# Kernel tuning notes

Hardware: AMD Instinct MI355X
Metric: run time of the kernel (lower is better)

Reference implementation:

```python
import jax, jax.numpy as jnp
import numpy as np

NEG_INF = -1e9  # mask fill value used by the original layer
LEAKY_SLOPE = 0.2


def setup_inputs() -> dict:
    key = jax.random.key(0)
    k1, k2, k3, k4 = jax.random.split(key, 4)
    B, N, D_in = 8, 1024, 256
    H, head_dim = 8, 32  # output_dim=256, concat_heads=True
    node_features = jax.random.normal(k1, (B, N, D_in), dtype=jnp.float32)
    adjacency = jax.random.randint(k2, (B, N, N), 0, 2, dtype=jnp.int32)
    W = jax.random.normal(k3, (H, D_in, head_dim), dtype=jnp.float32) * (1.0 / np.sqrt(D_in))
    a = jax.random.normal(k4, (H, 2 * head_dim), dtype=jnp.float32) * (1.0 / np.sqrt(2 * head_dim))
    bias = jnp.zeros((H * head_dim,), dtype=jnp.float32)
    return {"node_features": node_features, "adjacency": adjacency, "W": W, "a": a, "bias": bias}


def reference(node_features, adjacency, W, a, bias):
    # node_features: (B,N,D_in); adjacency: (B,N,N) in {0,1}
    H, _, hd = W.shape
    # Per-head linear transform: (B,H,N,head_dim)
    Wh = jnp.einsum('bni,hij->bhnj', node_features, W)
    # a @ concat(h_i, h_j) == a1 @ h_i + a2 @ h_j  (avoids O(N^2*2hd) concat)
    a1, a2 = a[:, :hd], a[:, hd:]
    e_i = jnp.einsum('bhnj,hj->bhn', Wh, a1)  # (B,H,N) source term
    e_j = jnp.einsum('bhnj,hj->bhn', Wh, a2)  # (B,H,N) target term
    scores = e_i[:, :, :, None] + e_j[:, :, None, :]  # (B,H,N,N)
    # LeakyReLU(0.2) exactly as ops.maximum(x, 0.2*x)
    scores = jnp.maximum(scores, LEAKY_SLOPE * scores)
    mask = adjacency.astype(scores.dtype)[:, None, :, :]  # (B,1,N,N)
    masked = scores * mask + (1.0 - mask) * NEG_INF
    attn = jax.nn.softmax(masked, axis=-1)  # (B,H,N,N)
    attended = jnp.einsum('bhij,bhjk->bhik', attn, Wh)  # (B,H,N,hd)
    B, _, N, _ = attended.shape
    # concat heads -> (B,N,H*hd); head order matches the python loop concat
    out = attended.transpose(0, 2, 1, 3).reshape(B, N, H * hd)
    out = out + bias
    return jax.nn.relu(out)
```

## Files before the change

### kernel.cpp

```cpp
#include <hip/hip_runtime.h>

#define GAT_B   8
#define GAT_N   1024
#define GAT_DIN 256
#define GAT_H   8
#define GAT_HD  32
#define GAT_LOG2E 1.4426950408889634f

typedef unsigned short gu16;
typedef unsigned int   gu32;
typedef __bf16 bf16x8 __attribute__((ext_vector_type(8)));
typedef __bf16 bf16x4 __attribute__((ext_vector_type(4)));
typedef float  f32x4v __attribute__((ext_vector_type(4)));

#if __has_builtin(__builtin_amdgcn_exp2f)
#define GAT_EXP2(x) __builtin_amdgcn_exp2f(x)
#else
#define GAT_EXP2(x) exp2f(x)
#endif

__device__ __forceinline__ float gb2f(gu16 u) { return __uint_as_float(((gu32)u) << 16); }

__device__ __forceinline__ void gat_detect(const gu16* p, int t, int* sflag) {
    if (t < 64) {
        int e0 = (p[2 * t]     >> 7) & 0xFF;
        int e1 = (p[2 * t + 1] >> 7) & 0xFF;
        unsigned long long m = __ballot((e0 >= 140) || (e1 >= 140));
        if (t == 0) *sflag = (m != 0ULL);
    }
}

__global__ __launch_bounds__(512) void CustomGATLayer_90348932038855_kernel(
    const void* __restrict__ Xv, const void* __restrict__ Wv, const void* __restrict__ Av,
    __bf16* __restrict__ whb, float* __restrict__ e1, float* __restrict__ e2)
{
    __shared__ __align__(16) __bf16 WlF[GAT_DIN * GAT_HD];
    __shared__ int sflag;

    const int t  = threadIdx.x;
    const int id = blockIdx.x;
    const int h  = id >> 5;
    const int mg = id & 31;

    gat_detect((const gu16*)Xv, t, &sflag);
    __syncthreads();
    const int fp32 = sflag;

    if (fp32) {
        const float* ws = (const float*)Wv + (size_t)h * GAT_DIN * GAT_HD;
        #pragma unroll
        for (int q = 0; q < 4; ++q) {
            int idx = q * 2048 + t * 4;
            int i = idx >> 5, k = idx & 31;
            float4 v = *(const float4*)(ws + idx);
            int d = (((i >> 5) * 32 + k) * 4 + ((i >> 3) & 3)) * 8 + (i & 7);
            WlF[d] = (__bf16)v.x; WlF[d + 32] = (__bf16)v.y;
            WlF[d + 64] = (__bf16)v.z; WlF[d + 96] = (__bf16)v.w;
        }
    } else {
        const gu16* ws = (const gu16*)Wv + (size_t)h * GAT_DIN * GAT_HD;
        gu16* wl = (gu16*)WlF;
        #pragma unroll
        for (int q = 0; q < 4; ++q) {
            int idx = q * 2048 + t * 4;
            int i = idx >> 5, k = idx & 31;
            ushort4 v = *(const ushort4*)(ws + idx);
            int d = (((i >> 5) * 32 + k) * 4 + ((i >> 3) & 3)) * 8 + (i & 7);
            wl[d] = v.x; wl[d + 32] = v.y; wl[d + 64] = v.z; wl[d + 96] = v.w;
        }
    }
    __syncthreads();

    const int wid = t >> 6, l = t & 63, g = l >> 4, c = l & 15;

    bf16x8 bf0[8], bf1[8];
    #pragma unroll
    for (int kc = 0; kc < 8; ++kc) {
        bf0[kc] = *(const bf16x8*)&WlF[((kc * 32 + c) * 4 + g) * 8];
        bf1[kc] = *(const bf16x8*)&WlF[((kc * 32 + c + 16) * 4 + g) * 8];
    }

    float a1c, a1c16, a2c, a2c16;
    if (fp32) {
        const float* ap = (const float*)Av + h * 2 * GAT_HD;
        a1c = ap[c] * GAT_LOG2E;      a1c16 = ap[c + 16] * GAT_LOG2E;
        a2c = ap[32 + c] * GAT_LOG2E; a2c16 = ap[48 + c] * GAT_LOG2E;
    } else {
        const gu16* ap = (const gu16*)Av + h * 2 * GAT_HD;
        a1c = gb2f(ap[c]) * GAT_LOG2E;      a1c16 = gb2f(ap[c + 16]) * GAT_LOG2E;
        a2c = gb2f(ap[32 + c]) * GAT_LOG2E; a2c16 = gb2f(ap[48 + c]) * GAT_LOG2E;
    }

    #pragma unroll
    for (int tt = 0; tt < 2; ++tt) {
        const int mt   = mg * 16 + wid * 2 + tt;
        const int M0   = mt * 16;
        const int b    = M0 >> 10;
        const int nloc = M0 & 1023;
        const int row  = nloc + c;

        f32x4v acc0 = {0.f, 0.f, 0.f, 0.f};
        f32x4v acc1 = {0.f, 0.f, 0.f, 0.f};

        if (fp32) {
            const float* xb = (const float*)Xv + ((size_t)b * GAT_N + row) * GAT_DIN;
            #pragma unroll
            for (int kc = 0; kc < 8; ++kc) {
                float4 x0 = *(const float4*)(xb + kc * 32 + 8 * g);
                float4 x1 = *(const float4*)(xb + kc * 32 + 8 * g + 4);
                bf16x8 af;
                af[0] = (__bf16)x0.x; af[1] = (__bf16)x0.y; af[2] = (__bf16)x0.z; af[3] = (__bf16)x0.w;
                af[4] = (__bf16)x1.x; af[5] = (__bf16)x1.y; af[6] = (__bf16)x1.z; af[7] = (__bf16)x1.w;
                acc0 = __builtin_amdgcn_mfma_f32_16x16x32_bf16(af, bf0[kc], acc0, 0, 0, 0);
                acc1 = __builtin_amdgcn_mfma_f32_16x16x32_bf16(af, bf1[kc], acc1, 0, 0, 0);
            }
        } else {
            const gu16* xb = (const gu16*)Xv + ((size_t)b * GAT_N + row) * GAT_DIN;
            #pragma unroll
            for (int kc = 0; kc < 8; ++kc) {
                bf16x8 af = *(const bf16x8*)(xb + kc * 32 + 8 * g);
                acc0 = __builtin_amdgcn_mfma_f32_16x16x32_bf16(af, bf0[kc], acc0, 0, 0, 0);
                acc1 = __builtin_amdgcn_mfma_f32_16x16x32_bf16(af, bf1[kc], acc1, 0, 0, 0);
            }
        }

        const int nb = nloc + 4 * g;
        const int jcc = nb >> 5, kg = (nb >> 3) & 3, e0 = nb & 7;
        const size_t fb = (((size_t)(b * GAT_H + h) * 32 + jcc) * 4 + kg) * 32;
        bf16x4 v0, v1;
        v0[0] = (__bf16)acc0[0]; v0[1] = (__bf16)acc0[1];
        v0[2] = (__bf16)acc0[2]; v0[3] = (__bf16)acc0[3];
        v1[0] = (__bf16)acc1[0]; v1[1] = (__bf16)acc1[1];
        v1[2] = (__bf16)acc1[2]; v1[3] = (__bf16)acc1[3];
        *(bf16x4*)(whb + (fb + c) * 8 + e0)      = v0;
        *(bf16x4*)(whb + (fb + c + 16) * 8 + e0) = v1;

        float p1[4], p2[4];
        #pragma unroll
        for (int q = 0; q < 4; ++q) {
            p1[q] = acc0[q] * a1c + acc1[q] * a1c16;
            p2[q] = acc0[q] * a2c + acc1[q] * a2c16;
            #pragma unroll
            for (int mm = 1; mm <= 8; mm <<= 1) {
                p1[q] += __shfl_xor(p1[q], mm);
                p2[q] += __shfl_xor(p2[q], mm);
            }
        }
        if (c == 0) {
            const size_t eb = (size_t)(b * GAT_H + h) * GAT_N + nb;
            #pragma unroll
            for (int q = 0; q < 4; ++q) { e1[eb + q] = p1[q]; e2[eb + q] = p2[q]; }
        }
    }
}

__global__ __launch_bounds__(512) void CustomGATLayer_90348932038855_attn(
    const void* __restrict__ Xv, const int* __restrict__ adj, const void* __restrict__ biasv,
    const __bf16* __restrict__ whb, const float* __restrict__ e1f, const float* __restrict__ e2f,
    float* __restrict__ out)
{
    __shared__ __align__(16) float e2l[GAT_H * GAT_N];
    __shared__ int sflag;

    const int t = threadIdx.x;
    const int h = t >> 6, l = t & 63, g = l >> 4, c = l & 15;
    const int id = blockIdx.x;
    const int b = id & 7, tile = id >> 3;
    const int i0 = tile * 16;

    gat_detect((const gu16*)Xv, t, &sflag);

    {
        const float* s = e2f + (size_t)(b * GAT_H + h) * GAT_N;
        float* d = e2l + h * GAT_N;
        #pragma unroll
        for (int q = 0; q < 4; ++q) {
            int off = (q * 64 + l) * 4;
            *(float4*)(d + off) = *(const float4*)(s + off);
        }
    }
    __syncthreads();
    const int fp32 = sflag;

    const float e1r = e1f[(size_t)(b * GAT_H + h) * GAT_N + i0 + c];
    const int* adjr = adj + ((size_t)(b * GAT_N + i0 + c)) * GAT_N + 8 * g;
    const __bf16* whr = whb + (size_t)(b * GAT_H + h) * (GAT_N * GAT_HD) + g * 256 + c * 8;
    const float* e2h = e2l + h * GAT_N + 8 * g;

    int4 aA0 = *(const int4*)(adjr),      aA1 = *(const int4*)(adjr + 4);
    int4 aB0 = *(const int4*)(adjr + 32), aB1 = *(const int4*)(adjr + 36);
    int4 aC0 = *(const int4*)(adjr + 64), aC1 = *(const int4*)(adjr + 68);
    bf16x8 wA0 = *(const bf16x8*)(whr),        wA1 = *(const bf16x8*)(whr + 128);
    bf16x8 wB0 = *(const bf16x8*)(whr + 1024), wB1 = *(const bf16x8*)(whr + 1152);

    f32x4v acc0 = {0.f, 0.f, 0.f, 0.f};
    f32x4v acc1 = {0.f, 0.f, 0.f, 0.f};
    f32x4v accS = {0.f, 0.f, 0.f, 0.f};
    bf16x8 onesf;
    #pragma unroll
    for (int e = 0; e < 8; ++e) onesf[e] = (__bf16)1.0f;

#define GAT_WCOMP(EV, AV, IDX) {                    \
        float s_ = e1r + (EV);                      \
        s_ = fmaxf(s_, 0.2f * s_);                  \
        s_ = fminf(s_, 86.0f);                      \
        float w_ = GAT_EXP2(s_);                    \
        w_ = (AV) ? w_ : 0.0f;                      \
        pf[IDX] = (__bf16)w_; }

    #pragma unroll 2
    for (int jc = 0; jc < 32; ++jc) {
        const int4 a0 = aA0, a1 = aA1;
        const bf16x8 w0 = wA0, w1 = wA1;
        aA0 = aB0; aA1 = aB1; aB0 = aC0; aB1 = aC1;
        wA0 = wB0; wA1 = wB1;
        if (jc < 29) {
            const int* an = adjr + (jc + 3) * 32;
            aC0 = *(const int4*)an; aC1 = *(const int4*)(an + 4);
        }
        if (jc < 30) {
            const __bf16* wn = whr + (jc + 2) * 1024;
            wB0 = *(const bf16x8*)wn; wB1 = *(const bf16x8*)(wn + 128);
        }
        float4 ea = *(const float4*)(e2h + jc * 32);
        float4 eb = *(const float4*)(e2h + jc * 32 + 4);
        bf16x8 pf;
        GAT_WCOMP(ea.x, a0.x, 0) GAT_WCOMP(ea.y, a0.y, 1)
        GAT_WCOMP(ea.z, a0.z, 2) GAT_WCOMP(ea.w, a0.w, 3)
        GAT_WCOMP(eb.x, a1.x, 4) GAT_WCOMP(eb.y, a1.y, 5)
        GAT_WCOMP(eb.z, a1.z, 6) GAT_WCOMP(eb.w, a1.w, 7)
        acc0 = __builtin_amdgcn_mfma_f32_16x16x32_bf16(pf, w0, acc0, 0, 0, 0);
        acc1 = __builtin_amdgcn_mfma_f32_16x16x32_bf16(pf, w1, acc1, 0, 0, 0);
        accS = __builtin_amdgcn_mfma_f32_16x16x32_bf16(pf, onesf, accS, 0, 0, 0);
    }
#undef GAT_WCOMP

    float bv0, bv1;
    if (fp32) {
        const float* bp = (const float*)biasv + h * GAT_HD;
        bv0 = bp[c]; bv1 = bp[c + 16];
    } else {
        const gu16* bp = (const gu16*)biasv + h * GAT_HD;
        bv0 = gb2f(bp[c]); bv1 = gb2f(bp[c + 16]);
    }

    float* ob = out + (size_t)(b * GAT_N + i0) * (GAT_H * GAT_HD) + h * GAT_HD + c;
    #pragma unroll
    for (int q = 0; q < 4; ++q) {
        float d = accS[q];
        float r = (d > 0.f) ? (1.0f / d) : 0.0f;
        float o0 = fmaxf(acc0[q] * r + bv0, 0.f);
        float o1 = fmaxf(acc1[q] * r + bv1, 0.f);
        ob[(size_t)(4 * g + q) * (GAT_H * GAT_HD)]      = o0;
        ob[(size_t)(4 * g + q) * (GAT_H * GAT_HD) + 16] = o1;
    }
}

extern "C" void kernel_launch(void* const* d_in, const int* in_sizes, int n_in,
                              void* d_out, int out_size, void* d_ws, size_t ws_size,
                              hipStream_t stream) {
    const void* X    = d_in[0];
    const int*  adj  = (const int*)d_in[1];
    const void* Wm   = d_in[2];
    const void* Av   = d_in[3];
    const void* bias = d_in[4];
    float* outp = (float*)d_out;

    __bf16* whb = (__bf16*)d_ws;
    float* e1 = (float*)(whb + (size_t)GAT_B * GAT_H * GAT_N * GAT_HD);
    float* e2 = e1 + (size_t)GAT_B * GAT_H * GAT_N;

    CustomGATLayer_90348932038855_kernel
        <<<dim3(8 * 32), 512, 0, stream>>>(X, Wm, Av, whb, e1, e2);
    CustomGATLayer_90348932038855_attn
        <<<dim3((GAT_N / 16) * GAT_B), 512, 0, stream>>>(
            X, adj, bias, whb, e1, e2, outp);
}
```

Baseline: 134.3 us.

## Pack adjacency into bitmasks in a prep kernel and restructure projection kernel

Adds a pre-pass kernel that converts the int32 adjacency matrix into 64-bit ballot bitmasks and pre-swizzles W into bf16 fragment layout in global memory. The attention kernel then reads a small bitmask tile into shared memory instead of streaming the full int32 adjacency once per head-wave. The projection kernel is also reorganised so each block handles 16 rows across all heads, staging X in LDS and reading W fragments from global. Cost: an extra launch and a full pass over adjacency, though it is read once instead of eight times (once per head).

```diff
diff --git a/kernel.cpp b/kernel.cpp
--- a/kernel.cpp
+++ b/kernel.cpp
@@ -9,6 +9,7 @@
 
 typedef unsigned short gu16;
 typedef unsigned int   gu32;
+typedef unsigned long long gu64;
 typedef __bf16 bf16x8 __attribute__((ext_vector_type(8)));
 typedef __bf16 bf16x4 __attribute__((ext_vector_type(4)));
 typedef float  f32x4v __attribute__((ext_vector_type(4)));
@@ -30,55 +31,111 @@
     }
 }
 
+__global__ __launch_bounds__(512) void CustomGATLayer_90348932038855_pack(
+    const void* __restrict__ Xv, const int* __restrict__ adj, const void* __restrict__ Wv,
+    gu64* __restrict__ pk, __bf16* __restrict__ wfg)
+{
+    __shared__ int sflag;
+    const int t = threadIdx.x, bid = blockIdx.x;
+    gat_detect((const gu16*)Xv, t, &sflag);
+    __syncthreads();
+    const int fp32 = sflag;
+
+    if (bid < 8) {
+        const int h = bid;
+        if (fp32) {
+            const float* ws = (const float*)Wv + (size_t)h * 8192;
+            #pragma unroll
+            for (int q = 0; q < 4; ++q) {
+                int idx = q * 2048 + t * 4;
+                int i = idx >> 5, k = idx & 31;
+                float4 v = *(const float4*)(ws + idx);
+                int d = h * 8192 + (((i >> 5) * 32 + k) * 4 + ((i >> 3) & 3)) * 8 + (i & 7);
+                wfg[d] = (__bf16)v.x; wfg[d + 32] = (__bf16)v.y;
+                wfg[d + 64] = (__bf16)v.z; wfg[d + 96] = (__bf16)v.w;
+            }
+        } else {
+            const gu16* ws = (const gu16*)Wv + (size_t)h * 8192;
+            gu16* wo = (gu16*)wfg;
+            #pragma unroll
+            for (int q = 0; q < 4; ++q) {
+                int idx = q * 2048 + t * 4;
+                int i = idx >> 5, k = idx & 31;
+                ushort4 v = *(const ushort4*)(ws + idx);
+                int d = h * 8192 + (((i >> 5) * 32 + k) * 4 + ((i >> 3) & 3)) * 8 + (i & 7);
+                wo[d] = v.x; wo[d + 32] = v.y; wo[d + 64] = v.z; wo[d + 96] = v.w;
+            }
+        }
+    }
+
+    const int w = t >> 6, l = t & 63;
+    const int r0 = bid * 32 + w * 4;
+    for (int r = 0; r < 4; ++r) {
+        const int* ar = adj + (size_t)(r0 + r) * GAT_N;
+        gu64* po = pk + (size_t)(r0 + r) * 16;
+        #pragma unroll
+        for (int s = 0; s < 16; ++s) {
+            int v = ar[s * 64 + l];
+            gu64 m = __ballot(v != 0);
+            if (l == 0) po[s] = m;
+        }
+    }
+}
+
 __global__ __launch_bounds__(512) void CustomGATLayer_90348932038855_kernel(
-    const void* __restrict__ Xv, const void* __restrict__ Wv, const void* __restrict__ Av,
+    const void* __restrict__ Xv, const __bf16* __restrict__ wfg, const void* __restrict__ Av,
     __bf16* __restrict__ whb, float* __restrict__ e1, float* __restrict__ e2)
 {
-    __shared__ __align__(16) __bf16 WlF[GAT_DIN * GAT_HD];
+    __shared__ __align__(16) __bf16 Xl[16][264];
     __shared__ int sflag;
 
-    const int t  = threadIdx.x;
-    const int id = blockIdx.x;
-    const int h  = id >> 5;
-    const int mg = id & 31;
-
+    const int t = threadIdx.x;
     gat_detect((const gu16*)Xv, t, &sflag);
+
+    const int bt = blockIdx.x;
+    const int M0 = bt * 16, b = M0 >> 10, nloc = M0 & 1023;
+    const int srow = t >> 5, scol = (t & 31) * 8;
     __syncthreads();
     const int fp32 = sflag;
 
     if (fp32) {
-        const float* ws = (const float*)Wv + (size_t)h * GAT_DIN * GAT_HD;
-        #pragma unroll
-        for (int q = 0; q < 4; ++q) {
-            int idx = q * 2048 + t * 4;
-            int i = idx >> 5, k = idx & 31;
-            float4 v = *(const float4*)(ws + idx);
-            int d = (((i >> 5) * 32 + k) * 4 + ((i >> 3) & 3)) * 8 + (i & 7);
-            WlF[d] = (__bf16)v.x; WlF[d + 32] = (__bf16)v.y;
-            WlF[d + 64] = (__bf16)v.z; WlF[d + 96] = (__bf16)v.w;
-        }
+        const float* xs = (const float*)Xv + ((size_t)(b * GAT_N + nloc + srow)) * GAT_DIN + scol;
+        float4 x0 = *(const float4*)(xs);
+        float4 x1 = *(const float4*)(xs + 4);
+        bf16x8 xv;
+        xv[0] = (__bf16)x0.x; xv[1] = (__bf16)x0.y; xv[2] = (__bf16)x0.z; xv[3] = (__bf16)x0.w;
+        xv[4] = (__bf16)x1.x; xv[5] = (__bf16)x1.y; xv[6] = (__bf16)x1.z; xv[7] = (__bf16)x1.w;
+        *(bf16x8*)&Xl[srow][scol] = xv;
     } else {
-        const gu16* ws = (const gu16*)Wv + (size_t)h * GAT_DIN * GAT_HD;
-        gu16* wl = (gu16*)WlF;
-        #pragma unroll
-        for (int q = 0; q < 4; ++q) {
-            int idx = q * 2048 + t * 4;
-            int i = idx >> 5, k = idx & 31;
-            ushort4 v = *(const ushort4*)(ws + idx);
-            int d = (((i >> 5) * 32 + k) * 4 + ((i >> 3) & 3)) * 8 + (i & 7);
-            wl[d] = v.x; wl[d + 32] = v.y; wl[d + 64] = v.z; wl[d + 96] = v.w;
-        }
-    }
-    __syncthreads();
-
-    const int wid = t >> 6, l = t & 63, g = l >> 4, c = l & 15;
-
-    bf16x8 bf0[8], bf1[8];
+        const gu16* xs = (const gu16*)Xv + ((size_t)(b * GAT_N + nloc + srow)) * GAT_DIN + scol;
+        *(bf16x8*)&Xl[srow][scol] = *(const bf16x8*)xs;
+    }
+    __syncthreads();
+
+    const int h = t >> 6, l = t & 63, g = l >> 4, c = l & 15;
+    const __bf16* wf = wfg + h * 8192;
+
+    f32x4v acc0 = {0.f, 0.f, 0.f, 0.f};
+    f32x4v acc1 = {0.f, 0.f, 0.f, 0.f};
     #pragma unroll
     for (int kc = 0; kc < 8; ++kc) {
-        bf0[kc] = *(const bf16x8*)&WlF[((kc * 32 + c) * 4 + g) * 8];
-        bf1[kc] = *(const bf16x8*)&WlF[((kc * 32 + c + 16) * 4 + g) * 8];
-    }
+        bf16x8 af = *(const bf16x8*)&Xl[c][kc * 32 + 8 * g];
+        bf16x8 b0 = *(const bf16x8*)(wf + ((kc * 32 + c) * 4 + g) * 8);
+        bf16x8 b1 = *(const bf16x8*)(wf + ((kc * 32 + c + 16) * 4 + g) * 8);
+        acc0 = __builtin_amdgcn_mfma_f32_16x16x32_bf16(af, b0, acc0, 0, 0, 0);
+        acc1 = __builtin_amdgcn_mfma_f32_16x16x32_bf16(af, b1, acc1, 0, 0, 0);
+    }
+
+    const int nb = nloc + 4 * g;
+    const int jcc = nb >> 5, kg = (nb >> 3) & 3, e0 = nb & 7;
+    const size_t fb = (((size_t)(b * GAT_H + h) * 32 + jcc) * 4 + kg) * 32;
+    bf16x4 v0, v1;
+    v0[0] = (__bf16)acc0[0]; v0[1] = (__bf16)acc0[1];
+    v0[2] = (__bf16)acc0[2]; v0[3] = (__bf16)acc0[3];
+    v1[0] = (__bf16)acc1[0]; v1[1] = (__bf16)acc1[1];
+    v1[2] = (__bf16)acc1[2]; v1[3] = (__bf16)acc1[3];
+    *(bf16x4*)(whb + (fb + c) * 8 + e0)      = v0;
+    *(bf16x4*)(whb + (fb + c + 16) * 8 + e0) = v1;
 
     float a1c, a1c16, a2c, a2c16;
     if (fp32) {
@@ -90,76 +147,31 @@
         a1c = gb2f(ap[c]) * GAT_LOG2E;      a1c16 = gb2f(ap[c + 16]) * GAT_LOG2E;
         a2c = gb2f(ap[32 + c]) * GAT_LOG2E; a2c16 = gb2f(ap[48 + c]) * GAT_LOG2E;
     }
-
-    #pragma unroll
-    for (int tt = 0; tt < 2; ++tt) {
-        const int mt   = mg * 16 + wid * 2 + tt;
-        const int M0   = mt * 16;
-        const int b    = M0 >> 10;
-        const int nloc = M0 & 1023;
-        const int row  = nloc + c;
-
-        f32x4v acc0 = {0.f, 0.f, 0.f, 0.f};
-        f32x4v acc1 = {0.f, 0.f, 0.f, 0.f};
-
-        if (fp32) {
-            const float* xb = (const float*)Xv + ((size_t)b * GAT_N + row) * GAT_DIN;
-            #pragma unroll
-            for (int kc = 0; kc < 8; ++kc) {
-                float4 x0 = *(const float4*)(xb + kc * 32 + 8 * g);
-                float4 x1 = *(const float4*)(xb + kc * 32 + 8 * g + 4);
-                bf16x8 af;
-                af[0] = (__bf16)x0.x; af[1] = (__bf16)x0.y; af[2] = (__bf16)x0.z; af[3] = (__bf16)x0.w;
-                af[4] = (__bf16)x1.x; af[5] = (__bf16)x1.y; af[6] = (__bf16)x1.z; af[7] = (__bf16)x1.w;
-                acc0 = __builtin_amdgcn_mfma_f32_16x16x32_bf16(af, bf0[kc], acc0, 0, 0, 0);
-                acc1 = __builtin_amdgcn_mfma_f32_16x16x32_bf16(af, bf1[kc], acc1, 0, 0, 0);
-            }
-        } else {
-            const gu16* xb = (const gu16*)Xv + ((size_t)b * GAT_N + row) * GAT_DIN;
-            #pragma unroll
-            for (int kc = 0; kc < 8; ++kc) {
-                bf16x8 af = *(const bf16x8*)(xb + kc * 32 + 8 * g);
-                acc0 = __builtin_amdgcn_mfma_f32_16x16x32_bf16(af, bf0[kc], acc0, 0, 0, 0);
-                acc1 = __builtin_amdgcn_mfma_f32_16x16x32_bf16(af, bf1[kc], acc1, 0, 0, 0);
-            }
-        }
-
-        const int nb = nloc + 4 * g;
-        const int jcc = nb >> 5, kg = (nb >> 3) & 3, e0 = nb & 7;
-        const size_t fb = (((size_t)(b * GAT_H + h) * 32 + jcc) * 4 + kg) * 32;
-        bf16x4 v0, v1;
-        v0[0] = (__bf16)acc0[0]; v0[1] = (__bf16)acc0[1];
-        v0[2] = (__bf16)acc0[2]; v0[3] = (__bf16)acc0[3];
-        v1[0] = (__bf16)acc1[0]; v1[1] = (__bf16)acc1[1];
-        v1[2] = (__bf16)acc1[2]; v1[3] = (__bf16)acc1[3];
-        *(bf16x4*)(whb + (fb + c) * 8 + e0)      = v0;
-        *(bf16x4*)(whb + (fb + c + 16) * 8 + e0) = v1;
-
-        float p1[4], p2[4];
-        #pragma unroll
-        for (int q = 0; q < 4; ++q) {
-            p1[q] = acc0[q] * a1c + acc1[q] * a1c16;
-            p2[q] = acc0[q] * a2c + acc1[q] * a2c16;
-            #pragma unroll
-            for (int mm = 1; mm <= 8; mm <<= 1) {
-                p1[q] += __shfl_xor(p1[q], mm);
-                p2[q] += __shfl_xor(p2[q], mm);
-            }
-        }
-        if (c == 0) {
-            const size_t eb = (size_t)(b * GAT_H + h) * GAT_N + nb;
-            #pragma unroll
-            for (int q = 0; q < 4; ++q) { e1[eb + q] = p1[q]; e2[eb + q] = p2[q]; }
-        }
+    float p1[4], p2[4];
+    #pragma unroll
+    for (int q = 0; q < 4; ++q) {
+        p1[q] = acc0[q] * a1c + acc1[q] * a1c16;
+        p2[q] = acc0[q] * a2c + acc1[q] * a2c16;
+        #pragma unroll
+        for (int mm = 1; mm <= 8; mm <<= 1) {
+            p1[q] += __shfl_xor(p1[q], mm);
+            p2[q] += __shfl_xor(p2[q], mm);
+        }
+    }
+    if (c == 0) {
+        const size_t eb = (size_t)(b * GAT_H + h) * GAT_N + nb;
+        #pragma unroll
+        for (int q = 0; q < 4; ++q) { e1[eb + q] = p1[q]; e2[eb + q] = p2[q]; }
     }
 }
 
 __global__ __launch_bounds__(512) void CustomGATLayer_90348932038855_attn(
-    const void* __restrict__ Xv, const int* __restrict__ adj, const void* __restrict__ biasv,
+    const void* __restrict__ Xv, const gu32* __restrict__ pk32, const void* __restrict__ biasv,
     const __bf16* __restrict__ whb, const float* __restrict__ e1f, const float* __restrict__ e2f,
     float* __restrict__ out)
 {
     __shared__ __align__(16) float e2l[GAT_H * GAT_N];
+    __shared__ gu32 pkl[16][33];
     __shared__ int sflag;
 
     const int t = threadIdx.x;
@@ -171,6 +183,10 @@
     gat_detect((const gu16*)Xv, t, &sflag);
 
     {
+        const int prow = t >> 5, pjc = t & 31;
+        pkl[prow][pjc] = pk32[((size_t)(b * GAT_N + i0 + prow)) * 32 + pjc];
+    }
+    {
         const float* s = e2f + (size_t)(b * GAT_H + h) * GAT_N;
         float* d = e2l + h * GAT_N;
         #pragma unroll
@@ -183,13 +199,9 @@
     const int fp32 = sflag;
 
     const float e1r = e1f[(size_t)(b * GAT_H + h) * GAT_N + i0 + c];
-    const int* adjr = adj + ((size_t)(b * GAT_N + i0 + c)) * GAT_N + 8 * g;
     const __bf16* whr = whb + (size_t)(b * GAT_H + h) * (GAT_N * GAT_HD) + g * 256 + c * 8;
     const float* e2h = e2l + h * GAT_N + 8 * g;
 
-    int4 aA0 = *(const int4*)(adjr),      aA1 = *(const int4*)(adjr + 4);
-    int4 aB0 = *(const int4*)(adjr + 32), aB1 = *(const int4*)(adjr + 36);
-    int4 aC0 = *(const int4*)(adjr + 64), aC1 = *(const int4*)(adjr + 68);
     bf16x8 wA0 = *(const bf16x8*)(whr),        wA1 = *(const bf16x8*)(whr + 128);
     bf16x8 wB0 = *(const bf16x8*)(whr + 1024), wB1 = *(const bf16x8*)(whr + 1152);
 
@@ -200,35 +212,30 @@
     #pragma unroll
     for (int e = 0; e < 8; ++e) onesf[e] = (__bf16)1.0f;
 
-#define GAT_WCOMP(EV, AV, IDX) {                    \
+#define GAT_WCOMP(EV, IDX) {                        \
         float s_ = e1r + (EV);                      \
         s_ = fmaxf(s_, 0.2f * s_);                  \
         s_ = fminf(s_, 86.0f);                      \
         float w_ = GAT_EXP2(s_);                    \
-        w_ = (AV) ? w_ : 0.0f;                      \
+        w_ = (ab & (1u << IDX)) ? w_ : 0.0f;        \
         pf[IDX] = (__bf16)w_; }
 
     #pragma unroll 2
     for (int jc = 0; jc < 32; ++jc) {
-        const int4 a0 = aA0, a1 = aA1;
         const bf16x8 w0 = wA0, w1 = wA1;
-        aA0 = aB0; aA1 = aB1; aB0 = aC0; aB1 = aC1;
         wA0 = wB0; wA1 = wB1;
-        if (jc < 29) {
-            const int* an = adjr + (jc + 3) * 32;
-            aC0 = *(const int4*)an; aC1 = *(const int4*)(an + 4);
-        }
         if (jc < 30) {
             const __bf16* wn = whr + (jc + 2) * 1024;
             wB0 = *(const bf16x8*)wn; wB1 = *(const bf16x8*)(wn + 128);
         }
+        const gu32 ab = (pkl[c][jc] >> (8 * g)) & 0xFFu;
         float4 ea = *(const float4*)(e2h + jc * 32);
         float4 eb = *(const float4*)(e2h + jc * 32 + 4);
         bf16x8 pf;
-        GAT_WCOMP(ea.x, a0.x, 0) GAT_WCOMP(ea.y, a0.y, 1)
-        GAT_WCOMP(ea.z, a0.z, 2) GAT_WCOMP(ea.w, a0.w, 3)
-        GAT_WCOMP(eb.x, a1.x, 4) GAT_WCOMP(eb.y, a1.y, 5)
-        GAT_WCOMP(eb.z, a1.z, 6) GAT_WCOMP(eb.w, a1.w, 7)
+        GAT_WCOMP(ea.x, 0) GAT_WCOMP(ea.y, 1)
+        GAT_WCOMP(ea.z, 2) GAT_WCOMP(ea.w, 3)
+        GAT_WCOMP(eb.x, 4) GAT_WCOMP(eb.y, 5)
+        GAT_WCOMP(eb.z, 6) GAT_WCOMP(eb.w, 7)
         acc0 = __builtin_amdgcn_mfma_f32_16x16x32_bf16(pf, w0, acc0, 0, 0, 0);
         acc1 = __builtin_amdgcn_mfma_f32_16x16x32_bf16(pf, w1, acc1, 0, 0, 0);
         accS = __builtin_amdgcn_mfma_f32_16x16x32_bf16(pf, onesf, accS, 0, 0, 0);
@@ -267,12 +274,16 @@
     float* outp = (float*)d_out;
 
     __bf16* whb = (__bf16*)d_ws;
-    float* e1 = (float*)(whb + (size_t)GAT_B * GAT_H * GAT_N * GAT_HD);
-    float* e2 = e1 + (size_t)GAT_B * GAT_H * GAT_N;
-
+    float* e1  = (float*)(whb + (size_t)GAT_B * GAT_H * GAT_N * GAT_HD);
+    float* e2  = e1 + (size_t)GAT_B * GAT_H * GAT_N;
+    __bf16* wfg = (__bf16*)(e2 + (size_t)GAT_B * GAT_H * GAT_N);
+    gu64* pk   = (gu64*)(wfg + (size_t)GAT_H * GAT_DIN * GAT_HD);
+
+    CustomGATLayer_90348932038855_pack
+        <<<dim3(256), 512, 0, stream>>>(X, adj, Wm, pk, wfg);
     CustomGATLayer_90348932038855_kernel
-        <<<dim3(8 * 32), 512, 0, stream>>>(X, Wm, Av, whb, e1, e2);
+        <<<dim3(512), 512, 0, stream>>>(X, wfg, Av, whb, e1, e2);
     CustomGATLayer_90348932038855_attn
         <<<dim3((GAT_N / 16) * GAT_B), 512, 0, stream>>>(
-            X, adj, bias, whb, e1, e2, outp);
-}
+            X, (const gu32*)pk, bias, whb, e1, e2, outp);
+}
```

After: 135.6 us. About the same (+0.9%).
